# Performance work log

Hardware: AMD Instinct MI355X
Metric: run time of the kernel (lower is better)

## Reference

```python
import math
import jax, jax.numpy as jnp
from jax import lax
import numpy as np

SIZE = 5      # kernel size == num_gaussian
MUL = 16      # multiplicity of 0e and 1o in irreps_in/out
IN_DIM = 4 * MUL  # 16 scalars + 16 vectors = 64


def real_sh(v, xp=jnp):
    """Real spherical harmonics l=0..3, component normalization (||Y_l||^2=2l+1
    on unit vectors), homogeneous polynomial form so the zero vector maps to
    (1,0,...,0). v: (...,3) -> (...,16)."""
    x = v[..., 0]; y = v[..., 1]; z = v[..., 2]
    r2 = x * x + y * y + z * z
    s3 = math.sqrt(3.0); s5 = math.sqrt(5.0); s15 = math.sqrt(15.0)
    s7 = math.sqrt(7.0); s105 = math.sqrt(105.0)
    c21 = 0.5 * math.sqrt(10.5)   # (1/2)sqrt(21/2)
    c35 = 0.5 * math.sqrt(17.5)   # (1/2)sqrt(35/2)
    out = [
        xp.ones_like(x),
        s3 * y, s3 * z, s3 * x,
        s15 * x * y, s15 * y * z, 0.5 * s5 * (3 * z * z - r2),
        s15 * x * z, 0.5 * s15 * (x * x - y * y),
        c35 * y * (3 * x * x - y * y), s105 * x * y * z,
        c21 * y * (5 * z * z - r2), 0.5 * s7 * z * (5 * z * z - 3 * r2),
        c21 * x * (5 * z * z - r2), 0.5 * s105 * z * (x * x - y * y),
        c35 * x * (x * x - 3 * y * y),
    ]
    return xp.stack(out, axis=-1)


def _wigner3j(l1, l2, l3, rng):
    """Unit-Frobenius-norm SO(3)-invariant 3-tensor in the real SH basis above,
    found as the nullspace of rotation-invariance constraints (fp64 numpy)."""
    dims = (2 * l1 + 1, 2 * l2 + 1, 2 * l3 + 1)
    n = dims[0] * dims[1] * dims[2]
    rows = []
    for _ in range(4):
        A = rng.standard_normal((3, 3))
        Q, _ = np.linalg.qr(A)
        if np.linalg.det(Q) < 0:
            Q = -Q
        X = rng.standard_normal((64, 3))
        X /= np.linalg.norm(X, axis=1, keepdims=True)
        YA = real_sh(X, np)
        YB = real_sh(X @ Q.T, np)
        Ds = []
        for l in (l1, l2, l3):
            sl = slice(l * l, (l + 1) * (l + 1))
            D = np.linalg.lstsq(YA[:, sl], YB[:, sl], rcond=None)[0].T
            Ds.append(D)
        rows.append(np.kron(Ds[0], np.kron(Ds[1], Ds[2])) - np.eye(n))
    _, _, Vt = np.linalg.svd(np.concatenate(rows, 0))
    w = Vt[-1]
    w = w * np.sign(w[np.argmax(np.abs(w))])  # deterministic sign
    w = w / np.linalg.norm(w)
    return w.reshape(dims).astype(np.float32)

_rng = np.random.default_rng(7)
W3J = {k: jnp.asarray(_wigner3j(*k, _rng))
       for k in [(0, 0, 0), (0, 1, 1), (1, 0, 1), (1, 1, 0), (1, 2, 1)]}


def setup_inputs() -> dict:
    key = jax.random.key(0)
    k1, k2, k3, k4 = jax.random.split(key, 4)
    return {
        "x": jax.random.normal(k1, (4, IN_DIM, 32, 32, 32), jnp.float32),
        "w_lin0": jax.random.normal(k2, (MUL, MUL), jnp.float32),
        "w_lin1": jax.random.normal(k3, (MUL, MUL), jnp.float32),
        "tp_weight": jax.random.normal(k4, (SIZE, 5 * MUL * MUL), jnp.float32),
    }


def reference(x, w_lin0, w_lin1, tp_weight):
    size, mul = SIZE, MUL
    # --- lattice buffers (d, sh) ---
    r = jnp.linspace(-1.0, 1.0, size)
    lat = jnp.stack(jnp.meshgrid(r, r, r, indexing="ij"), axis=-1)  # (s,s,s,3)
    d = jnp.sqrt(jnp.sum(lat * lat, axis=-1))
    v = lat / jnp.maximum(d, 1e-12)[..., None]
    sh = real_sh(v)  # (s,s,s,16)
    # --- gaussian radial basis -> per-voxel tp weights ---
    centers = jnp.linspace(0.0, 1.0, size)
    sigma = 1.0 / (size - 1)
    emb = jnp.exp(-jnp.square((d[..., None] - centers) / sigma)) / 1.12
    w = (emb @ tp_weight) * jnp.cos(jnp.pi * d)[..., None] / size ** 1.5
    W = w.reshape(size, size, size, 5, mul, mul)  # 5 tp instructions
    # path normalization: sqrt((2l_out+1)/fan_in), fan_in = sum mul1*mul2 per output
    f0 = math.sqrt(1.0 / (2 * mul))   # 0e output: 2 paths of fan 16
    f1 = math.sqrt(3.0 / (3 * mul))   # 1o output: 3 paths of fan 16

    def blk(C, ysl, Wp, f):
        # C: (2l1+1,2l2+1,2l3+1); ysl: (s,s,s,2l2+1); Wp: (s,s,s,mul,mul)
        t = f * jnp.einsum("abc,xyzb,xyzuw->xyzuawc", C, ysl, Wp)
        s = t.shape
        return t.reshape(size, size, size, s[3] * s[4], s[5] * s[6])

    y0 = sh[..., 0:1]; y1 = sh[..., 1:4]; y2 = sh[..., 4:9]
    b00 = blk(W3J[(0, 0, 0)], y0, W[..., 0, :, :], f0)   # 0e->0e (16,16)
    b01 = blk(W3J[(0, 1, 1)], y1, W[..., 1, :, :], f1)   # 0e->1o (16,48)
    b11a = blk(W3J[(1, 0, 1)], y0, W[..., 2, :, :], f1)  # 1o->1o (48,48)
    b10 = blk(W3J[(1, 1, 0)], y1, W[..., 3, :, :], f0)   # 1o->0e (48,16)
    b11b = blk(W3J[(1, 2, 1)], y2, W[..., 4, :, :], f1)  # 1o->1o (48,48)
    k = jnp.concatenate([
        jnp.concatenate([b00, b01], axis=-1),
        jnp.concatenate([b10, b11a + b11b], axis=-1)], axis=-2)  # (s,s,s,64,64)
    kernel = jnp.transpose(k, (4, 3, 0, 1, 2))  # oixyz
    # --- self-interaction (e3nn Linear, per-l block, 1/sqrt(fan_in)) ---
    B = x.shape[0]
    sp = x.shape[2:]
    inv = 1.0 / math.sqrt(mul)
    x0 = x[:, :mul]
    x1 = x[:, mul:].reshape(B, mul, 3, *sp)
    si0 = inv * jnp.einsum("uv,buxyz->bvxyz", w_lin0, x0)
    si1 = inv * jnp.einsum("uv,bumxyz->bvmxyz", w_lin1, x1)
    si = jnp.concatenate([si0, si1.reshape(B, 3 * mul, *sp)], axis=1)
    # --- conv3d (cross-correlation, padding size//2) ---
    conv = lax.conv_general_dilated(
        x, kernel, window_strides=(1, 1, 1),
        padding=[(size // 2, size // 2)] * 3,
        dimension_numbers=("NCDHW", "OIDHW", "NCDHW"))
    return si + 0.1 * conv
```

## Files before the change

kernel.cpp:

```cpp
#include <hip/hip_runtime.h>
#include <math.h>

typedef __attribute__((ext_vector_type(8))) short bf16x8;
typedef __attribute__((ext_vector_type(16))) float f32x16;
typedef __attribute__((ext_vector_type(4))) unsigned int u32x4;

#define XB 131072

__device__ __forceinline__ unsigned f2bf(float f) {
    union { float f; unsigned u; } v; v.f = f;
    return (v.u + 0x7FFFu + ((v.u >> 16) & 1u)) >> 16;
}

template<int VM6, int LG>
__device__ __forceinline__ void waitcnt_fence() {
    __builtin_amdgcn_s_waitcnt((VM6 & 15) | ((VM6 >> 4) << 14) | (7 << 4) | (LG << 8));
    __builtin_amdgcn_sched_barrier(0);
}

__global__ __launch_bounds__(256) void build_K(
    const float* __restrict__ w_lin0,
    const float* __restrict__ w_lin1,
    const float* __restrict__ tp_weight,
    unsigned short* __restrict__ Kb3)
{
    const int tid = (int)threadIdx.x;
    const int tap = (int)blockIdx.x;
#define KIDX(o, i) ((((i) >> 3) * 128 + tap) * 512 + (o) * 8 + ((i) & 7))
    if (tap >= 125) {
        for (int n = tid; n < 4096; n += 256)
            Kb3[(n >> 9) * 65536 + tap * 512 + (n & 511)] = 0;
        return;
    }
    const int i1 = tap / 25, i2 = (tap / 5) % 5, i3 = tap % 5;
    const float X = -1.0f + 0.5f * (float)i1;
    const float Y = -1.0f + 0.5f * (float)i2;
    const float Z = -1.0f + 0.5f * (float)i3;
    const float d = sqrtf(X*X + Y*Y + Z*Z);
    const float dinv = 1.0f / fmaxf(d, 1e-12f);
    const float vx = X * dinv, vy = Y * dinv, vz = Z * dinv;
    const float r2 = vx*vx + vy*vy + vz*vz;

    __shared__ float wsh[1280];
    __shared__ float y1s[3];
    __shared__ float Qs[9];

    if (tid == 0) {
        const float s3 = 1.7320508075688772f;
        const float s15 = 3.872983346207417f;
        y1s[0] = s3 * vy; y1s[1] = s3 * vz; y1s[2] = s3 * vx;
        float y2v0 = s15 * vx * vy;
        float y2v1 = s15 * vy * vz;
        float y2v2 = 1.118033988749895f * (3.0f * vz * vz - r2);
        float y2v3 = s15 * vx * vz;
        float y2v4 = 1.9364916731037085f * (vx * vx - vy * vy);
        const float INV10 = 0.31622776601683794f;
        const float INV30 = 0.18257418583505536f;
        Qs[0] = -y2v2 * INV30 - y2v4 * INV10;
        Qs[4] =  2.0f * y2v2 * INV30;
        Qs[8] = -y2v2 * INV30 + y2v4 * INV10;
        Qs[1] = Qs[3] = y2v1 * INV10;
        Qs[2] = Qs[6] = y2v0 * INV10;
        Qs[5] = Qs[7] = y2v3 * INV10;
    }

    float emb[5];
    #pragma unroll
    for (int e = 0; e < 5; ++e) {
        float t = (d - 0.25f * (float)e) * 4.0f;
        emb[e] = expf(-t * t) * (1.0f / 1.12f);
    }
    const float scale = cosf(3.14159265358979323846f * d) / 11.180339887498949f;

    for (int j = tid; j < 1280; j += 256) {
        float s = 0.0f;
        #pragma unroll
        for (int e = 0; e < 5; ++e) s += emb[e] * tp_weight[e * 1280 + j];
        wsh[j] = scale * s;
    }
    __syncthreads();

    const float F0   = 0.17677669529663687f;
    const float F1   = 0.25f;
    const float F0S3 = 0.10206207261596574f;
    const float F1S3 = 0.14433756729740646f;

    #pragma unroll 1
    for (int n = 0; n < 16; ++n) {
        int e = n * 256 + tid;
        int o = e & 63, i = e >> 6;
        float Kv;
        if (o < 16) {
            if (i < 16) {
                Kv = F0 * wsh[0 * 256 + i * 16 + o];
            } else {
                int u = (i - 16) / 3, a = (i - 16) % 3;
                Kv = F0S3 * y1s[a] * wsh[3 * 256 + u * 16 + o];
            }
        } else {
            int wcol = (o - 16) / 3, c = (o - 16) % 3;
            if (i < 16) {
                Kv = F1S3 * y1s[c] * wsh[1 * 256 + i * 16 + wcol];
            } else {
                int u = (i - 16) / 3, a = (i - 16) % 3;
                Kv = F1 * Qs[a * 3 + c] * wsh[4 * 256 + u * 16 + wcol];
                if (a == c) Kv += F1S3 * wsh[2 * 256 + u * 16 + wcol];
            }
        }
        if (tap == 62) {
            if (o < 16) {
                if (i < 16) Kv += 2.5f * w_lin0[i * 16 + o];
            } else if (i >= 16) {
                int v = (o - 16) / 3, m = (o - 16) % 3;
                int u = (i - 16) / 3, a = (i - 16) % 3;
                if (a == m) Kv += 2.5f * w_lin1[u * 16 + v];
            }
        }
        Kb3[KIDX(o, i)] = (unsigned short)f2bf(Kv);
    }
#undef KIDX
}

__global__ __launch_bounds__(256) void to_blc(
    const float* __restrict__ x,
    unsigned short* __restrict__ xbz)
{
    const int tid = (int)threadIdx.x, blk = (int)blockIdx.x;
    if (blk == 0 && tid < 64) xbz[tid] = 0;
    const int p = blk * 256 + tid;
    const int b = p >> 15, pos = p & 32767;
    const float* xp = x + ((size_t)b << 21) + pos;
    unsigned short* op = xbz + 64 + (size_t)p * 64;
    #pragma unroll
    for (int cg = 0; cg < 8; ++cg) {
        u32x4 dv;
        #pragma unroll
        for (int jj = 0; jj < 4; ++jj) {
            float f0 = xp[((size_t)(cg * 8 + 2 * jj)) << 15];
            float f1 = xp[((size_t)(cg * 8 + 2 * jj + 1)) << 15];
            dv[jj] = f2bf(f0) | (f2bf(f1) << 16);
        }
        *(u32x4*)(op + cg * 8) = dv;
    }
}

template<int P, int PLAST>
__device__ __forceinline__ void kstep2(
    const int (&nbase)[2], int abase, bool thv,
    bf16x8 (&Ar)[2][2], bf16x8 (&Br)[2][2], f32x16 (&acc)[2][2])
{
    if constexpr (P < PLAST) {
        constexpr int Q = P + 1;
        constexpr int t0 = 2 * Q;
        constexpr int t1 = (2 * Q + 1 == 125) ? 124 : 2 * Q + 1;
        constexpr int dA = ((t0 / 25) * 144 + ((t0 / 5) % 5) * 12 + (t0 % 5)) * 16;
        constexpr int dB = ((t1 / 25) * 144 + ((t1 / 5) % 5) * 12 + (t1 % 5)) * 16;
        #pragma unroll
        for (int mo = 0; mo < 2; ++mo) {
            int a = Q * 2048 + abase + mo * 512;
            asm volatile("ds_read_b128 %0, %1" : "=v"(Ar[Q & 1][mo]) : "v"(a));
        }
        int dsel = thv ? dB : dA;
        #pragma unroll
        for (int np = 0; np < 2; ++np) {
            int a = nbase[np] + dsel;
            asm volatile("ds_read_b128 %0, %1" : "=v"(Br[Q & 1][np]) : "v"(a));
        }
    }
    waitcnt_fence<63, (P < PLAST) ? 4 : 0>();
    #pragma unroll
    for (int mo = 0; mo < 2; ++mo)
        #pragma unroll
        for (int np = 0; np < 2; ++np)
            acc[mo][np] = __builtin_amdgcn_mfma_f32_32x32x16_bf16(
                Ar[P & 1][mo], Br[P & 1][np], acc[mo][np], 0, 0, 0);
    if constexpr (P < PLAST)
        kstep2<P + 1, PLAST>(nbase, abase, thv, Ar, Br, acc);
}

template<int P0, int PLAST>
__device__ __forceinline__ void runphase(
    const int (&nbase)[2], int abase, bool thv, f32x16 (&acc)[2][2])
{
    bf16x8 Ar[2][2], Br[2][2];
    constexpr int t0 = 2 * P0, t1 = 2 * P0 + 1;
    constexpr int dA = ((t0 / 25) * 144 + ((t0 / 5) % 5) * 12 + (t0 % 5)) * 16;
    constexpr int dB = ((t1 / 25) * 144 + ((t1 / 5) % 5) * 12 + (t1 % 5)) * 16;
    #pragma unroll
    for (int mo = 0; mo < 2; ++mo) {
        int a = P0 * 2048 + abase + mo * 512;
        asm volatile("ds_read_b128 %0, %1" : "=v"(Ar[P0 & 1][mo]) : "v"(a));
    }
    int dsel = thv ? dB : dA;
    #pragma unroll
    for (int np = 0; np < 2; ++np) {
        int a = nbase[np] + dsel;
        asm volatile("ds_read_b128 %0, %1" : "=v"(Br[P0 & 1][np]) : "v"(a));
    }
    kstep2<P0, PLAST>(nbase, abase, thv, Ar, Br, acc);
}

__global__ __launch_bounds__(512, 1) void conv_mfma(
    const unsigned short* __restrict__ xbz,
    const unsigned short* __restrict__ Kb3,
    float* __restrict__ out)
{
    __shared__ __align__(16) char lds[158720];

    const int tid = (int)threadIdx.x;
    const int blk = (int)blockIdx.x;
    const int xt = blk & 3, yt = (blk >> 2) & 3, zt = (blk >> 4) & 3, b = blk >> 6;
    const int lane = tid & 63, wv = tid >> 6;
    const int l31 = lane & 31;
    const bool thv = (lane >= 32);

    unsigned srcOff[4];
    int xdst[4];
    {
        const int gz0 = zt * 8 - 2, gy0 = yt * 8 - 2, gx0 = xt * 8 - 2;
        #pragma unroll
        for (int i = 0; i < 4; ++i) {
            int c = tid + i * 512;
            if (c >= 1728) c -= 1728;
            int hz = c / 144; int rem = c - hz * 144;
            int hy = rem / 12;  int hx = rem - hy * 12;
            int gz = gz0 + hz, gy = gy0 + hy, gx = gx0 + hx;
            bool ok = ((unsigned)gz < 32u) && ((unsigned)gy < 32u) && ((unsigned)gx < 32u);
            int pg = (gz << 10) + (gy << 5) + gx;
            srcOff[i] = ok ? (unsigned)(128 + (((b << 15) + pg) << 7)) : 0u;
            xdst[i] = XB + c * 16;
        }
    }

    const int abase = l31 * 16 + (thv ? 1024 : 0);
    int nbase[2];
    #pragma unroll
    for (int np = 0; np < 2; ++np)
        nbase[np] = XB + ((wv * 12 + (l31 >> 3) + 4 * np) * 12 + (l31 & 7)) * 16;

    f32x16 acc[2][2];
    #pragma unroll
    for (int i = 0; i < 2; ++i)
        #pragma unroll
        for (int j = 0; j < 2; ++j) acc[i][j] = (f32x16)0.0f;

    const char* kb = (const char*)Kb3;
    const int kchunk = tid * 16;

    #pragma unroll
    for (int j = 0; j < 8; ++j) {
        __builtin_amdgcn_global_load_lds(
            (const __attribute__((address_space(1))) unsigned int*)(kb + kchunk + j * 8192),
            (__attribute__((address_space(3))) unsigned int*)(lds + kchunk + j * 8192),
            16, 0, 0);
    }

    #pragma unroll 1
    for (int s = 0; s < 8; ++s) {
        const char* kbs = kb + s * 131072;

        __builtin_amdgcn_s_barrier();
        __builtin_amdgcn_sched_barrier(0);
        #pragma unroll
        for (int i = 0; i < 4; ++i) {
            __builtin_amdgcn_global_load_lds(
                (const __attribute__((address_space(1))) unsigned int*)
                    ((const char*)xbz + srcOff[i] + s * 16),
                (__attribute__((address_space(3))) unsigned int*)(lds + xdst[i]),
                16, 0, 0);
        }
        #pragma unroll
        for (int j = 0; j < 8; ++j) {
            __builtin_amdgcn_global_load_lds(
                (const __attribute__((address_space(1))) unsigned int*)
                    (kbs + 65536 + kchunk + j * 8192),
                (__attribute__((address_space(3))) unsigned int*)
                    (lds + 65536 + kchunk + j * 8192),
                16, 0, 0);
        }
        waitcnt_fence<8, 15>();
        __builtin_amdgcn_s_barrier();
        __builtin_amdgcn_sched_barrier(0);

        runphase<0, 31>(nbase, abase, thv, acc);

        __builtin_amdgcn_s_barrier();
        __builtin_amdgcn_sched_barrier(0);
        #pragma unroll
        for (int j = 0; j < 8; ++j) {
            __builtin_amdgcn_global_load_lds(
                (const __attribute__((address_space(1))) unsigned int*)
                    (kbs + 131072 + kchunk + j * 8192),
                (__attribute__((address_space(3))) unsigned int*)
                    (lds + kchunk + j * 8192),
                16, 0, 0);
        }
        waitcnt_fence<8, 15>();
        __builtin_amdgcn_s_barrier();
        __builtin_amdgcn_sched_barrier(0);

        runphase<32, 62>(nbase, abase, thv, acc);
    }

    const int gz = zt * 8 + wv;
    #pragma unroll
    for (int mo = 0; mo < 2; ++mo) {
        #pragma unroll
        for (int np = 0; np < 2; ++np) {
            #pragma unroll
            for (int reg = 0; reg < 16; ++reg) {
                int o = mo * 32 + (reg & 3) + 8 * (reg >> 2) + (thv ? 4 : 0);
                int gy = yt * 8 + 4 * np + (l31 >> 3);
                int gx = xt * 8 + (l31 & 7);
                out[(((size_t)(b * 64 + o)) << 15) + (gz << 10) + (gy << 5) + gx] =
                    0.1f * acc[mo][np][reg];
            }
        }
    }
}

extern "C" void kernel_launch(void* const* d_in, const int* in_sizes, int n_in,
                              void* d_out, int out_size, void* d_ws, size_t ws_size,
                              hipStream_t stream) {
    const float* x       = (const float*)d_in[0];
    const float* w_lin0  = (const float*)d_in[1];
    const float* w_lin1  = (const float*)d_in[2];
    const float* tp      = (const float*)d_in[3];
    unsigned short* Kb3 = (unsigned short*)d_ws;
    unsigned short* xbz = (unsigned short*)((char*)d_ws + (2u << 20));
    float* out = (float*)d_out;

    build_K<<<128, 256, 0, stream>>>(w_lin0, w_lin1, tp, Kb3);
    to_blc<<<512, 256, 0, stream>>>(x, xbz);
    conv_mfma<<<256, 512, 0, stream>>>(xbz, Kb3, out);
}
```

Baseline: 144.7 us.

## Deepen LDS operand prefetch and stage input slab through registers

The MFMA inner loop moves from double to triple register buffering, so LDS fragment reads are issued two k-steps ahead and LDS latency is better hidden. The per-slab input loads no longer go straight into LDS with global_load_lds at the top of each iteration. Instead the next slab is fetched into registers with plain global loads during the current iteration and written to LDS with ds_write at the start of the next one. This takes global latency off the critical barrier path, at the cost of more VGPRs. The vmcnt thresholds for waiting on outstanding loads change as well, so ordering correctness depends on exact counter accounting.

Measured after the change: 158.1 us. 1.09x slower.

```diff
diff --git a/kernel.cpp b/kernel.cpp
--- a/kernel.cpp
+++ b/kernel.cpp
@@ -147,10 +147,10 @@
 template<int P, int PLAST>
 __device__ __forceinline__ void kstep2(
     const int (&nbase)[2], int abase, bool thv,
-    bf16x8 (&Ar)[2][2], bf16x8 (&Br)[2][2], f32x16 (&acc)[2][2])
-{
-    if constexpr (P < PLAST) {
-        constexpr int Q = P + 1;
+    bf16x8 (&Ar)[3][2], bf16x8 (&Br)[3][2], f32x16 (&acc)[2][2])
+{
+    if constexpr (P + 2 <= PLAST) {
+        constexpr int Q = P + 2;
         constexpr int t0 = 2 * Q;
         constexpr int t1 = (2 * Q + 1 == 125) ? 124 : 2 * Q + 1;
         constexpr int dA = ((t0 / 25) * 144 + ((t0 / 5) % 5) * 12 + (t0 % 5)) * 16;
@@ -158,22 +158,23 @@
         #pragma unroll
         for (int mo = 0; mo < 2; ++mo) {
             int a = Q * 2048 + abase + mo * 512;
-            asm volatile("ds_read_b128 %0, %1" : "=v"(Ar[Q & 1][mo]) : "v"(a));
+            asm volatile("ds_read_b128 %0, %1" : "=v"(Ar[Q % 3][mo]) : "v"(a));
         }
         int dsel = thv ? dB : dA;
         #pragma unroll
         for (int np = 0; np < 2; ++np) {
             int a = nbase[np] + dsel;
-            asm volatile("ds_read_b128 %0, %1" : "=v"(Br[Q & 1][np]) : "v"(a));
-        }
-    }
-    waitcnt_fence<63, (P < PLAST) ? 4 : 0>();
+            asm volatile("ds_read_b128 %0, %1" : "=v"(Br[Q % 3][np]) : "v"(a));
+        }
+    }
+    constexpr int LG = (P + 2 <= PLAST) ? 8 : (P + 1 <= PLAST) ? 4 : 0;
+    waitcnt_fence<63, LG>();
     #pragma unroll
     for (int mo = 0; mo < 2; ++mo)
         #pragma unroll
         for (int np = 0; np < 2; ++np)
             acc[mo][np] = __builtin_amdgcn_mfma_f32_32x32x16_bf16(
-                Ar[P & 1][mo], Br[P & 1][np], acc[mo][np], 0, 0, 0);
+                Ar[P % 3][mo], Br[P % 3][np], acc[mo][np], 0, 0, 0);
     if constexpr (P < PLAST)
         kstep2<P + 1, PLAST>(nbase, abase, thv, Ar, Br, acc);
 }
@@ -182,20 +183,23 @@
 __device__ __forceinline__ void runphase(
     const int (&nbase)[2], int abase, bool thv, f32x16 (&acc)[2][2])
 {
-    bf16x8 Ar[2][2], Br[2][2];
-    constexpr int t0 = 2 * P0, t1 = 2 * P0 + 1;
-    constexpr int dA = ((t0 / 25) * 144 + ((t0 / 5) % 5) * 12 + (t0 % 5)) * 16;
-    constexpr int dB = ((t1 / 25) * 144 + ((t1 / 5) % 5) * 12 + (t1 % 5)) * 16;
-    #pragma unroll
-    for (int mo = 0; mo < 2; ++mo) {
-        int a = P0 * 2048 + abase + mo * 512;
-        asm volatile("ds_read_b128 %0, %1" : "=v"(Ar[P0 & 1][mo]) : "v"(a));
-    }
-    int dsel = thv ? dB : dA;
-    #pragma unroll
-    for (int np = 0; np < 2; ++np) {
-        int a = nbase[np] + dsel;
-        asm volatile("ds_read_b128 %0, %1" : "=v"(Br[P0 & 1][np]) : "v"(a));
+    bf16x8 Ar[3][2], Br[3][2];
+    #pragma unroll
+    for (int q = 0; q < 2; ++q) {
+        const int t0 = 2 * (P0 + q), t1 = 2 * (P0 + q) + 1;
+        const int dA = ((t0 / 25) * 144 + ((t0 / 5) % 5) * 12 + (t0 % 5)) * 16;
+        const int dB = ((t1 / 25) * 144 + ((t1 / 5) % 5) * 12 + (t1 % 5)) * 16;
+        #pragma unroll
+        for (int mo = 0; mo < 2; ++mo) {
+            int a = (P0 + q) * 2048 + abase + mo * 512;
+            asm volatile("ds_read_b128 %0, %1" : "=v"(Ar[(P0 + q) % 3][mo]) : "v"(a));
+        }
+        int dsel = thv ? dB : dA;
+        #pragma unroll
+        for (int np = 0; np < 2; ++np) {
+            int a = nbase[np] + dsel;
+            asm volatile("ds_read_b128 %0, %1" : "=v"(Br[(P0 + q) % 3][np]) : "v"(a));
+        }
     }
     kstep2<P0, PLAST>(nbase, abase, thv, Ar, Br, acc);
 }
@@ -254,6 +258,16 @@
             (__attribute__((address_space(3))) unsigned int*)(lds + kchunk + j * 8192),
             16, 0, 0);
     }
+    #pragma unroll
+    for (int i = 0; i < 4; ++i) {
+        __builtin_amdgcn_global_load_lds(
+            (const __attribute__((address_space(1))) unsigned int*)
+                ((const char*)xbz + srcOff[i]),
+            (__attribute__((address_space(3))) unsigned int*)(lds + xdst[i]),
+            16, 0, 0);
+    }
+
+    u32x4 xr[4];
 
     #pragma unroll 1
     for (int s = 0; s < 8; ++s) {
@@ -261,13 +275,11 @@
 
         __builtin_amdgcn_s_barrier();
         __builtin_amdgcn_sched_barrier(0);
-        #pragma unroll
-        for (int i = 0; i < 4; ++i) {
-            __builtin_amdgcn_global_load_lds(
-                (const __attribute__((address_space(1))) unsigned int*)
-                    ((const char*)xbz + srcOff[i] + s * 16),
-                (__attribute__((address_space(3))) unsigned int*)(lds + xdst[i]),
-                16, 0, 0);
+        if (s > 0) {
+            waitcnt_fence<8, 15>();
+            #pragma unroll
+            for (int i = 0; i < 4; ++i)
+                asm volatile("ds_write_b128 %0, %1" :: "v"(xdst[i]), "v"(xr[i]));
         }
         #pragma unroll
         for (int j = 0; j < 8; ++j) {
@@ -278,7 +290,16 @@
                     (lds + 65536 + kchunk + j * 8192),
                 16, 0, 0);
         }
-        waitcnt_fence<8, 15>();
+        {
+            unsigned sx = (unsigned)(((s < 7) ? s + 1 : 7) * 16);
+            #pragma unroll
+            for (int i = 0; i < 4; ++i) {
+                unsigned voff = srcOff[i] + sx;
+                asm volatile("global_load_dwordx4 %0, %1, %2"
+                             : "=v"(xr[i]) : "v"(voff), "s"(xbz));
+            }
+        }
+        waitcnt_fence<12, 0>();
         __builtin_amdgcn_s_barrier();
         __builtin_amdgcn_sched_barrier(0);
 
@@ -295,7 +316,7 @@
                     (lds + kchunk + j * 8192),
                 16, 0, 0);
         }
-        waitcnt_fence<8, 15>();
+        waitcnt_fence<12, 15>();
         __builtin_amdgcn_s_barrier();
         __builtin_amdgcn_sched_barrier(0);
 
```
